# Kernel optimization log

Hardware: AMD Instinct MI355X
Metric: run time of the kernel (lower is better)

## Reference

```python
import jax, jax.numpy as jnp
import numpy as np

B, N, H, FD = 2, 512, 128, 5
NT, SD, L = 3, 4, 3
COPY = 10.0
EPS = 1e-6


def setup_inputs() -> dict:
    key = jax.random.key(0)
    ks = jax.random.split(key, 20)
    node_type = jax.random.randint(ks[0], (B, N, 1), 0, NT).astype(jnp.float32)
    node_state = jax.random.normal(ks[1], (B, N, SD), jnp.float32)
    node_feats = jnp.concatenate([node_type, node_state], axis=-1)  # [B,N,5]
    adj = jax.random.bernoulli(ks[2], 0.05, (B, N, N)).astype(jnp.float32)
    adj = jnp.maximum(adj, adj.transpose(0, 2, 1)) * (1.0 - jnp.eye(N, dtype=jnp.float32))
    scope_node_mask = jax.random.bernoulli(ks[3], 0.5, (B, N)).astype(jnp.float32)
    scope_edge_mask = jax.random.bernoulli(ks[4], 0.5, (B, N, N)).astype(jnp.float32)
    s = 0.02
    p = dict(
        node_feats=node_feats, adj=adj,
        scope_node_mask=scope_node_mask, scope_edge_mask=scope_edge_mask,
        W_in=jax.random.normal(ks[5], (FD, H)) * s, b_in=jnp.zeros((H,)),
        W_mp=jax.random.normal(ks[6], (L, 2 * H, H)) * s, b_mp=jnp.zeros((L, H)),
        Wt1=jax.random.normal(ks[7], (H, H)) * s, bt1=jnp.zeros((H,)),
        Wt2=jax.random.normal(ks[8], (H, NT)) * s, bt2=jnp.zeros((NT,)),
        Ws1=jax.random.normal(ks[9], (H, H)) * s, bs1=jnp.zeros((H,)),
        Ws2=jax.random.normal(ks[10], (H, SD)) * s, bs2=jnp.zeros((SD,)),
        We1=jax.random.normal(ks[11], (4 * H, H)) * s, be1=jnp.zeros((H,)),
        We2=jax.random.normal(ks[12], (H, 3)) * s, be2=jnp.zeros((3,)),
    )
    return p


def _decode_edge_logits(adj, edl, eye):
    probs = jax.nn.softmax(edl, axis=-1)
    p_keep = probs[..., 0]  # EDGE_DELTA_KEEP = 0
    p_add = probs[..., 1]   # EDGE_DELTA_ADD = 1
    cur = (adj > 0.5).astype(edl.dtype)
    p_next = jnp.clip(p_add + p_keep * cur, EPS, 1.0 - EPS)
    el = jnp.log(p_next) - jnp.log1p(-p_next)  # logit
    return jnp.where(eye[None], -1e9, el)


def _forward(node_feats, adj, scope_node_mask, scope_edge_mask,
             W_in, b_in, W_mp, b_mp, Wt1, bt1, Wt2, bt2,
             Ws1, bs1, Ws2, bs2, We1, be1, We2, be2):
    # encoder: input proj + L rounds of [h, adj@h] -> Linear -> ReLU
    h = jax.nn.relu(node_feats @ W_in + b_in)  # [B,N,H]
    for l in range(L):
        msg = jnp.einsum('bij,bjh->bih', adj, h)
        h = jax.nn.relu(jnp.concatenate([h, msg], axis=-1) @ W_mp[l] + b_mp[l])
    # node heads (2-layer MLPs)
    type_local = jax.nn.relu(h @ Wt1 + bt1) @ Wt2 + bt2      # [B,N,NT]
    state_local = jax.nn.relu(h @ Ws1 + bs1) @ Ws2 + bs2     # [B,N,SD]
    # pairwise edge-delta head
    h_i = h[:, :, None, :]
    h_j = h[:, None, :, :]
    pair = jnp.concatenate([
        jnp.broadcast_to(h_i, (B, N, N, H)),
        jnp.broadcast_to(h_j, (B, N, N, H)),
        jnp.abs(h_i - h_j),
        h_i * h_j,
    ], axis=-1)  # [B,N,N,4H]
    edl = jax.nn.relu(pair @ We1 + be1) @ We2 + be2  # [B,N,N,3]
    edl = 0.5 * (edl + edl.transpose(0, 2, 1, 3))
    eye = jnp.eye(N, dtype=bool)
    edl = jnp.where(eye[None, :, :, None], 0.0, edl)
    # merges with copy paths
    cur_type = jnp.clip(node_feats[..., 0].astype(jnp.int32), 0, NT - 1)
    copy_type = jnp.where(jnp.arange(NT) == cur_type[..., None], COPY, -COPY)
    type_full = jnp.where(scope_node_mask[..., None] != 0, type_local, copy_type)
    scope = scope_node_mask[..., None]
    state_full = scope * state_local + (1.0 - scope) * node_feats[..., 1:]
    copy_edl = jnp.broadcast_to(jnp.where(jnp.arange(3) == 0, COPY, -COPY), (B, N, N, 3))
    copy_edl = jnp.where(eye[None, :, :, None], 0.0, copy_edl)
    edl_full = jnp.where(scope_edge_mask[..., None] != 0, edl, copy_edl)
    el_full = _decode_edge_logits(adj, edl_full, eye)
    return type_full, state_full, edl_full, el_full


def reference(node_feats, adj, scope_node_mask, scope_edge_mask,
              W_in, b_in, W_mp, b_mp, Wt1, bt1, Wt2, bt2,
              Ws1, bs1, Ws2, bs2, We1, be1, We2, be2):
    return _forward(node_feats, adj, scope_node_mask, scope_edge_mask,
                    W_in, b_in, W_mp, b_mp, Wt1, bt1, Wt2, bt2,
                    Ws1, bs1, Ws2, bs2, We1, be1, We2, be2)
```

## Files before the change

kernel.cpp:

```cpp
#include <hip/hip_runtime.h>
#include <hip/hip_fp16.h>
#include <math.h>

#define B_ 2
#define N_ 512
#define H_ 128
#define NT_ 3
#define SD_ 4
#define FD_ 5

typedef float f32x4 __attribute__((ext_vector_type(4)));
typedef unsigned int u32x4 __attribute__((ext_vector_type(4)));

#define MFMA4(a0, a1, a2, a3, av, b0, b1, b2, b3) \
    asm("s_nop 1\n\t" \
        "v_mfma_f32_16x16x32_f16 %0, %4, %5, %0\n\t" \
        "v_mfma_f32_16x16x32_f16 %1, %4, %6, %1\n\t" \
        "v_mfma_f32_16x16x32_f16 %2, %4, %7, %2\n\t" \
        "v_mfma_f32_16x16x32_f16 %3, %4, %8, %3" \
        : "+v"(a0), "+v"(a1), "+v"(a2), "+v"(a3) \
        : "v"(av), "v"(b0), "v"(b1), "v"(b2), "v"(b3))

#define MFMA16F(acc, a, b) \
    asm("s_nop 1\n\tv_mfma_f32_16x16x32_f16 %0, %1, %2, %0" \
        : "+v"(acc) : "v"(a), "v"(b))

#define PKMUL(d, a, b) \
    asm("v_pk_mul_f16 %0, %1, %2" : "=v"(d) : "v"(a), "v"(b))
#define PKSUB(d, a, b) \
    asm("v_pk_add_f16 %0, %1, %2 neg_lo:[0,1] neg_hi:[0,1]" \
        : "=v"(d) : "v"(a), "v"(b))
#define CVTPKF16(d, a, b) \
    asm("v_cvt_pkrtz_f16_f32 %0, %1, %2" : "=v"(d) : "v"(a), "v"(b))

static __device__ inline unsigned short f2h(float f) {
    return __half_as_ushort(__float2half(f));
}

__global__ __launch_bounds__(128) void k_input(const float* __restrict__ feats,
                                               const float* __restrict__ W_in,
                                               const float* __restrict__ b_in,
                                               float* __restrict__ hout,
                                               const float* __restrict__ We1,
                                               const float* __restrict__ We2,
                                               unsigned short* __restrict__ wfrag,
                                               unsigned short* __restrict__ wfrag2) {
    int blk = blockIdx.x, tid = threadIdx.x;
    if (blk < B_ * N_) {
        const float* f = feats + (size_t)blk * FD_;
        float acc = b_in[tid];
#pragma unroll
        for (int k = 0; k < FD_; ++k) acc += f[k] * W_in[k * H_ + tid];
        hout[(size_t)blk * H_ + tid] = fmaxf(acc, 0.f);
        return;
    }
    if (blk < B_ * N_ + 32) {
        int t = (blk - B_ * N_) * 128 + tid;
        int lane = t & 63, cg = (t >> 6) & 7, kb = t >> 9;
        int lr = lane & 15, g = lane >> 4;
        int c = cg * 16 + lr;
        unsigned o[4];
#pragma unroll
        for (int p = 0; p < 4; ++p) {
            float a = We1[(size_t)(256 + kb * 32 + 8 * g + 2 * p) * H_ + c];
            float bq = We1[(size_t)(256 + kb * 32 + 8 * g + 2 * p + 1) * H_ + c];
            o[p] = (unsigned)f2h(a) | ((unsigned)f2h(bq) << 16);
        }
        u32x4 v = {o[0], o[1], o[2], o[3]};
        *(u32x4*)(wfrag + (size_t)t * 8) = v;
        return;
    }
    {
        int t = (blk - (B_ * N_ + 32)) * 128 + tid;
        if (t < 256) {
            int kb = t >> 6, lane = t & 63;
            int oc = lane & 15, g = lane >> 4;
            unsigned w[4];
#pragma unroll
            for (int p = 0; p < 4; ++p) {
                int k0 = kb * 32 + g * 8 + 2 * p;
                int k1 = k0 + 1;
                int c0 = ((k0 >> 6) << 6) | ((k0 & 3) << 4) | ((k0 & 63) >> 2);
                int c1 = ((k1 >> 6) << 6) | ((k1 & 3) << 4) | ((k1 & 63) >> 2);
                float v0 = (oc < 3) ? We2[c0 * 3 + oc] : 0.f;
                float v1 = (oc < 3) ? We2[c1 * 3 + oc] : 0.f;
                w[p] = (unsigned)f2h(v0) | ((unsigned)f2h(v1) << 16);
            }
            u32x4 v = {w[0], w[1], w[2], w[3]};
            *(u32x4*)(wfrag2 + (size_t)t * 8) = v;
        }
    }
}

__global__ __launch_bounds__(128) void k_mp(const float* __restrict__ hin,
                                            float* __restrict__ hout,
                                            const float* __restrict__ adj,
                                            const float* __restrict__ Wl,
                                            const float* __restrict__ bl) {
    __shared__ float hi[H_];
    __shared__ float msg[H_];
    __shared__ unsigned short idxs[N_];
    __shared__ float avals[N_];
    __shared__ int cnt2[2];
    int node = blockIdx.x;
    int b = node >> 9;
    int tid = threadIdx.x;
    int w = tid >> 6, lane = tid & 63;
    hi[tid] = hin[(size_t)node * H_ + tid];
    const float* arow = adj + (size_t)node * N_;
    float4 av = ((const float4*)arow)[tid];
    int segbase = w * 256;
    int cum = 0;
#pragma unroll
    for (int q = 0; q < 4; ++q) {
        float a = (&av.x)[q];
        bool pred = (a != 0.f);
        unsigned long long mask = __ballot(pred);
        if (pred) {
            int pos = segbase + cum +
                      (int)__popcll(mask & ((1ull << lane) - 1ull));
            idxs[pos] = (unsigned short)(tid * 4 + q);
            avals[pos] = a;
        }
        cum += (int)__popcll(mask);
    }
    if (lane == 0) cnt2[w] = cum;
    __syncthreads();

    float m = 0.f;
    const float* hb = hin + ((size_t)b * N_) * H_;
    int n0 = cnt2[0], n1 = cnt2[1];
    for (int t = 0; t < n0; ++t)
        m += avals[t] * hb[(size_t)idxs[t] * H_ + tid];
    for (int t = 0; t < n1; ++t)
        m += avals[256 + t] * hb[(size_t)idxs[256 + t] * H_ + tid];
    msg[tid] = m;
    __syncthreads();

    float acc = bl[tid];
#pragma unroll 4
    for (int k = 0; k < H_; ++k) {
        acc += hi[k]  * Wl[(size_t)k * H_ + tid];
        acc += msg[k] * Wl[(size_t)(k + H_) * H_ + tid];
    }
    hout[(size_t)node * H_ + tid] = fmaxf(acc, 0.f);
}

__global__ __launch_bounds__(128) void k_heads(
    const float* __restrict__ h, const float* __restrict__ feats,
    const float* __restrict__ snm,
    const float* __restrict__ Wt1, const float* __restrict__ bt1,
    const float* __restrict__ Wt2, const float* __restrict__ bt2,
    const float* __restrict__ Ws1, const float* __restrict__ bs1,
    const float* __restrict__ Ws2, const float* __restrict__ bs2,
    const float* __restrict__ We1, const float* __restrict__ be1,
    float* __restrict__ Acoef, float* __restrict__ Bcoef,
    unsigned short* __restrict__ hf16,
    float* __restrict__ type_out, float* __restrict__ state_out) {
    __shared__ float hi[H_], hT[H_], hS[H_];
    int node = blockIdx.x, tid = threadIdx.x;
    float hv0 = h[(size_t)node * H_ + tid];
    hi[tid] = hv0;
    hf16[(size_t)node * H_ + tid] = f2h(hv0);
    __syncthreads();
    float at = bt1[tid], as = bs1[tid], aa = be1[tid], ab = 0.f;
#pragma unroll 4
    for (int k = 0; k < H_; ++k) {
        float hv = hi[k];
        at += hv * Wt1[k * H_ + tid];
        as += hv * Ws1[k * H_ + tid];
        aa += hv * We1[k * H_ + tid];
        ab += hv * We1[(k + H_) * H_ + tid];
    }
    hT[tid] = fmaxf(at, 0.f);
    hS[tid] = fmaxf(as, 0.f);
    int c = tid;
    int kp = ((c >> 6) << 6) | ((c & 15) << 2) | ((c >> 4) & 3);
    Acoef[(size_t)node * H_ + kp] = aa;
    Bcoef[(size_t)node * H_ + kp] = ab;
    __syncthreads();
    float sm = snm[node];
    if (tid < NT_) {
        float tl = bt2[tid];
        for (int cc = 0; cc < H_; ++cc) tl += hT[cc] * Wt2[cc * NT_ + tid];
        int ct = (int)feats[(size_t)node * FD_];
        ct = ct < 0 ? 0 : (ct > NT_ - 1 ? NT_ - 1 : ct);
        float cv = (tid == ct) ? 10.f : -10.f;
        type_out[(size_t)node * NT_ + tid] = (sm != 0.f) ? tl : cv;
    }
    if (tid >= 64 && tid < 64 + SD_) {
        int s = tid - 64;
        float sl = bs2[s];
        for (int cc = 0; cc < H_; ++cc) sl += hS[cc] * Ws2[cc * SD_ + s];
        state_out[(size_t)node * SD_ + s] =
            sm * sl + (1.f - sm) * feats[(size_t)node * FD_ + 1 + s];
    }
}

__global__ __launch_bounds__(256, 2) void k_pair2(
    const unsigned short* __restrict__ hf16,
    const float* __restrict__ Acp, const float* __restrict__ Bcp,
    const unsigned short* __restrict__ wfrag,
    const unsigned short* __restrict__ wfrag2,
    const float* __restrict__ be2,
    float* __restrict__ edl_out) {

    __shared__ unsigned short tile[2][128][128];

    int bid = blockIdx.x;
    int b = 0, r = bid;
    if (r >= 1280) { b = 1; r -= 1280; }
    int jtile, i;
    if (r < 128)      { jtile = 0; i = r; }
    else if (r < 384) { jtile = 1; i = r - 128; }
    else if (r < 768) { jtile = 2; i = r - 384; }
    else              { jtile = 3; i = r - 768; }
    int JT0 = jtile << 7;
    int bN = b << 9;

    int tid = threadIdx.x;
    int wave = tid >> 6, lane = tid & 63;
    int jh = wave >> 1, ch = wave & 1;
    int lr = lane & 15, g = lane >> 4;

    u32x4 Bf[4][8];
#pragma unroll
    for (int ct = 0; ct < 4; ++ct)
#pragma unroll
        for (int kb = 0; kb < 8; ++kb)
            Bf[ct][kb] = *(const u32x4*)(wfrag +
                (((size_t)kb * 8 + (ch * 4 + ct)) * 64 + lane) * 8);

    const unsigned short* hirow = hf16 + (size_t)(bN + i) * H_;
    u32x4 him[4];
#pragma unroll
    for (int m = 0; m < 4; ++m)
        him[m] = *(const u32x4*)(hirow + 32 * m + 8 * g);

    f32x4 AcoI = *(const f32x4*)(Acp + (size_t)(bN + i) * H_ + ch * 64 + lr * 4);
    f32x4 BcoI = *(const f32x4*)(Bcp + (size_t)(bN + i) * H_ + ch * 64 + lr * 4);

    char* tb0 = (char*)&tile[0][0][0];
    char* tb1 = (char*)&tile[1][0][0];

#pragma unroll
    for (int jt = 0; jt < 4; ++jt) {
        int jloc0 = jh * 64 + jt * 16;
        const unsigned short* hjp =
            hf16 + (size_t)(bN + JT0 + jloc0 + lr) * H_ + 8 * g;
        u32x4 hjall[4];
#pragma unroll
        for (int m = 0; m < 4; ++m)
            hjall[m] = *(const u32x4*)(hjp + 32 * m);
        f32x4 BcJv[4], AcJv[4];
#pragma unroll
        for (int rr = 0; rr < 4; ++rr) {
            size_t jn = (size_t)(bN + JT0 + jloc0 + 4 * g + rr) * H_ +
                        ch * 64 + lr * 4;
            BcJv[rr] = *(const f32x4*)(Bcp + jn);
            AcJv[rr] = *(const f32x4*)(Acp + jn);
        }

        f32x4 acc0 = {0.f,0.f,0.f,0.f}, acc1 = {0.f,0.f,0.f,0.f};
        f32x4 acc2 = {0.f,0.f,0.f,0.f}, acc3 = {0.f,0.f,0.f,0.f};

#pragma unroll
        for (int m = 0; m < 4; ++m) {
            u32x4 tav, uav;
#pragma unroll
            for (int p = 0; p < 4; ++p) {
                unsigned hip_ = him[m][p], hjp_ = hjall[m][p];
                unsigned u_, d_;
                PKMUL(u_, hip_, hjp_);
                PKSUB(d_, hip_, hjp_);
                uav[p] = u_;
                tav[p] = d_ & 0x7fff7fffu;
            }
            MFMA4(acc0, acc1, acc2, acc3, tav,
                  Bf[0][m], Bf[1][m], Bf[2][m], Bf[3][m]);
            MFMA4(acc0, acc1, acc2, acc3, uav,
                  Bf[0][4 + m], Bf[1][4 + m], Bf[2][4 + m], Bf[3][4 + m]);
        }
        asm("s_nop 7\n\ts_nop 7\n\ts_nop 3"
            : "+v"(acc0), "+v"(acc1), "+v"(acc2), "+v"(acc3));

#pragma unroll
        for (int rr = 0; rr < 4; ++rr) {
            int jloc = jloc0 + 4 * g + rr;
            float h10 = fmaxf(acc0[rr] + AcoI[0] + BcJv[rr][0], 0.f);
            float h11 = fmaxf(acc1[rr] + AcoI[1] + BcJv[rr][1], 0.f);
            float h12 = fmaxf(acc2[rr] + AcoI[2] + BcJv[rr][2], 0.f);
            float h13 = fmaxf(acc3[rr] + AcoI[3] + BcJv[rr][3], 0.f);
            float h20 = fmaxf(acc0[rr] + AcJv[rr][0] + BcoI[0], 0.f);
            float h21 = fmaxf(acc1[rr] + AcJv[rr][1] + BcoI[1], 0.f);
            float h22 = fmaxf(acc2[rr] + AcJv[rr][2] + BcoI[2], 0.f);
            float h23 = fmaxf(acc3[rr] + AcJv[rr][3] + BcoI[3], 0.f);
            unsigned w10, w11, w20, w21;
            CVTPKF16(w10, h10, h11); CVTPKF16(w11, h12, h13);
            CVTPKF16(w20, h20, h21); CVTPKF16(w21, h22, h23);
            int byte = jloc * 256 + ch * 128 + lr * 8;
            byte ^= (jloc & 7) << 4;
            uint2 v1; v1.x = w10; v1.y = w11;
            uint2 v2; v2.x = w20; v2.y = w21;
            *(uint2*)(tb0 + byte) = v1;
            *(uint2*)(tb1 + byte) = v2;
        }
    }

    u32x4 Bf2[4];
#pragma unroll
    for (int kb = 0; kb < 4; ++kb)
        Bf2[kb] = *(const u32x4*)(wfrag2 + ((size_t)kb * 64 + lane) * 8);

    __syncthreads();

    f32x4 pacc0 = {0.f,0.f,0.f,0.f}, pacc1 = {0.f,0.f,0.f,0.f};
    f32x4 pacc2 = {0.f,0.f,0.f,0.f}, pacc3 = {0.f,0.f,0.f,0.f};
#pragma unroll
    for (int p = 0; p < 4; ++p) {
        int f = wave + 4 * p;
        int orient = f >> 3, sub = f & 7;
        char* tb = orient ? tb1 : tb0;
        int jloc = sub * 16 + lr;
#pragma unroll
        for (int kb = 0; kb < 4; ++kb) {
            int byte = jloc * 256 + kb * 64 + g * 16;
            byte ^= (jloc & 7) << 4;
            u32x4 a = *(const u32x4*)(tb + byte);
            if (p == 0)      { MFMA16F(pacc0, a, Bf2[kb]); }
            else if (p == 1) { MFMA16F(pacc1, a, Bf2[kb]); }
            else if (p == 2) { MFMA16F(pacc2, a, Bf2[kb]); }
            else             { MFMA16F(pacc3, a, Bf2[kb]); }
        }
    }
    asm("s_nop 7\n\ts_nop 7\n\ts_nop 3"
        : "+v"(pacc0), "+v"(pacc1), "+v"(pacc2), "+v"(pacc3));
    __syncthreads();

    float* sbuf = (float*)&tile[0][0][0];
    if (lr < 3) {
#pragma unroll
        for (int p = 0; p < 4; ++p) {
            int f = wave + 4 * p;
            int orient = f >> 3, sub = f & 7;
            f32x4 pa = (p == 0) ? pacc0 : (p == 1) ? pacc1
                     : (p == 2) ? pacc2 : pacc3;
#pragma unroll
            for (int rr = 0; rr < 4; ++rr) {
                int jloc = sub * 16 + 4 * g + rr;
                sbuf[((orient << 7) + jloc) * 3 + lr] = pa[rr];
            }
        }
    }
    __syncthreads();

#pragma unroll
    for (int q = 0; q < 2; ++q) {
        int idx = q * 256 + tid;
        if (idx < 384) {
            int jloc = idx / 3, comp = idx - jloc * 3;
            float v = 0.5f * (sbuf[jloc * 3 + comp] +
                              sbuf[(128 + jloc) * 3 + comp]) + be2[comp];
            edl_out[((size_t)(bN + i) * N_ + (JT0 + jloc)) * 3 + comp] = v;
        }
    }
}

__global__ __launch_bounds__(256) void k_tr(float* __restrict__ edl,
                                            float* __restrict__ el,
                                            const float* __restrict__ sem,
                                            const float* __restrict__ adj) {
    __shared__ float ss[3][16][17];
    int tid = threadIdx.x;
    int r = tid >> 4, c = tid & 15;
    int bid = blockIdx.x;
    int b = 0, t = bid;
    if (t >= 528) { b = 1; t -= 528; }
    int J = (int)((sqrtf(8.f * (float)t + 1.f) - 1.f) * 0.5f);
    while ((J + 1) * (J + 2) / 2 <= t) ++J;
    while (J * (J + 1) / 2 > t) --J;
    int I = t - J * (J + 1) / 2;
    int i0 = I * 16, j0 = J * 16;
    int bN = b << 9;

    {
        const float* src = edl + ((size_t)(bN + i0 + r) * N_ + (j0 + c)) * 3;
        ss[0][r][c] = src[0];
        ss[1][r][c] = src[1];
        ss[2][r][c] = src[2];
    }
    __syncthreads();

    for (int pass = 0; pass < 2; ++pass) {
        if (pass == 1 && I == J) break;
        int gi, gj;
        float s0, s1, s2;
        if (I == J) {
            gi = i0 + r; gj = j0 + c;
            int lo = r <= c ? r : c, hi = r <= c ? c : r;
            s0 = ss[0][lo][hi]; s1 = ss[1][lo][hi]; s2 = ss[2][lo][hi];
        } else if (pass == 0) {
            gi = i0 + r; gj = j0 + c;
            s0 = ss[0][r][c]; s1 = ss[1][r][c]; s2 = ss[2][r][c];
        } else {
            gi = j0 + r; gj = i0 + c;
            s0 = ss[0][c][r]; s1 = ss[1][c][r]; s2 = ss[2][c][r];
        }
        size_t p = (size_t)(bN + gi) * N_ + gj;
        if (gi == gj) {
            edl[p * 3 + 0] = 0.f; edl[p * 3 + 1] = 0.f; edl[p * 3 + 2] = 0.f;
            el[p] = -1e9f;
        } else {
            float msk = sem[p];
            float e0 = (msk != 0.f) ? s0 : 10.f;
            float e1 = (msk != 0.f) ? s1 : -10.f;
            float e2 = (msk != 0.f) ? s2 : -10.f;
            edl[p * 3 + 0] = e0; edl[p * 3 + 1] = e1; edl[p * 3 + 2] = e2;
            float a = adj[p];
            float cur = (a > 0.5f) ? 1.f : 0.f;
            float mx = fmaxf(e0, fmaxf(e1, e2));
            float x0 = expf(e0 - mx), x1 = expf(e1 - mx), x2 = expf(e2 - mx);
            float inv = 1.f / (x0 + x1 + x2);
            float pn = x1 * inv + x0 * inv * cur;
            pn = fminf(fmaxf(pn, 1e-6f), 1.f - 1e-6f);
            el[p] = logf(pn) - log1pf(-pn);
        }
    }
}

extern "C" void kernel_launch(void* const* d_in, const int* in_sizes, int n_in,
                              void* d_out, int out_size, void* d_ws,
                              size_t ws_size, hipStream_t stream) {
    const float* feats = (const float*)d_in[0];
    const float* adj   = (const float*)d_in[1];
    const float* snm   = (const float*)d_in[2];
    const float* sem   = (const float*)d_in[3];
    const float* W_in  = (const float*)d_in[4];
    const float* b_in  = (const float*)d_in[5];
    const float* W_mp  = (const float*)d_in[6];
    const float* b_mp  = (const float*)d_in[7];
    const float* Wt1 = (const float*)d_in[8],  *bt1 = (const float*)d_in[9];
    const float* Wt2 = (const float*)d_in[10], *bt2 = (const float*)d_in[11];
    const float* Ws1 = (const float*)d_in[12], *bs1 = (const float*)d_in[13];
    const float* Ws2 = (const float*)d_in[14], *bs2 = (const float*)d_in[15];
    const float* We1 = (const float*)d_in[16], *be1 = (const float*)d_in[17];
    const float* We2 = (const float*)d_in[18], *be2 = (const float*)d_in[19];

    float* out = (float*)d_out;
    float* type_out  = out;
    float* state_out = out + 3072;
    float* edl_out   = out + 7168;
    float* el_out    = out + 7168 + 1572864;

    float* ws = (float*)d_ws;
    float* hA = ws;
    float* hB = ws + 131072;
    float* Bcp = ws + 262144;
    unsigned short* hf16   = (unsigned short*)(ws + 393216);
    unsigned short* wfrag  = (unsigned short*)(ws + 458752);
    unsigned short* wfrag2 = (unsigned short*)(ws + 475136);
    float* Acp = hA;

    k_input<<<B_ * N_ + 34, 128, 0, stream>>>(feats, W_in, b_in, hA,
                                              We1, We2, wfrag, wfrag2);
    k_mp<<<B_ * N_, H_, 0, stream>>>(hA, hB, adj,
                                     W_mp + 0 * 2 * H_ * H_, b_mp + 0 * H_);
    k_mp<<<B_ * N_, H_, 0, stream>>>(hB, hA, adj,
                                     W_mp + 1 * 2 * H_ * H_, b_mp + 1 * H_);
    k_mp<<<B_ * N_, H_, 0, stream>>>(hA, hB, adj,
                                     W_mp + 2 * 2 * H_ * H_, b_mp + 2 * H_);
    k_heads<<<B_ * N_, H_, 0, stream>>>(hB, feats, snm, Wt1, bt1, Wt2, bt2,
                                        Ws1, bs1, Ws2, bs2, We1, be1,
                                        Acp, Bcp, hf16, type_out, state_out);
    k_pair2<<<2560, 256, 0, stream>>>(hf16, Acp, Bcp, wfrag, wfrag2,
                                      be2, edl_out);
    k_tr<<<1056, 256, 0, stream>>>(edl_out, el_out, sem, adj);
}
```

Before: 128.8 us.

## Halve pair-kernel LDS tile by processing j in two 64-column halves, use builtins

The pair kernel now splits each 128-column j tile into two 64-column passes, cutting the shared fp16 tile from 64KB to 32KB and adding a small separate float reduction buffer. This is meant to let more blocks fit per CU. Inline-asm MFMA, packed f16 math and conversion macros are replaced with compiler builtins and vector f16 ops, so the compiler can schedule them and insert hazard waits itself. The second-layer weight fragments are loaded up front. The cost is extra __syncthreads per half and less work between barriers.

Result: no change. 128.4 us (-0.3%).

```diff
diff --git a/kernel.cpp b/kernel.cpp
--- a/kernel.cpp
+++ b/kernel.cpp
@@ -11,27 +11,16 @@
 
 typedef float f32x4 __attribute__((ext_vector_type(4)));
 typedef unsigned int u32x4 __attribute__((ext_vector_type(4)));
-
-#define MFMA4(a0, a1, a2, a3, av, b0, b1, b2, b3) \
-    asm("s_nop 1\n\t" \
-        "v_mfma_f32_16x16x32_f16 %0, %4, %5, %0\n\t" \
-        "v_mfma_f32_16x16x32_f16 %1, %4, %6, %1\n\t" \
-        "v_mfma_f32_16x16x32_f16 %2, %4, %7, %2\n\t" \
-        "v_mfma_f32_16x16x32_f16 %3, %4, %8, %3" \
-        : "+v"(a0), "+v"(a1), "+v"(a2), "+v"(a3) \
-        : "v"(av), "v"(b0), "v"(b1), "v"(b2), "v"(b3))
-
-#define MFMA16F(acc, a, b) \
-    asm("s_nop 1\n\tv_mfma_f32_16x16x32_f16 %0, %1, %2, %0" \
-        : "+v"(acc) : "v"(a), "v"(b))
-
-#define PKMUL(d, a, b) \
-    asm("v_pk_mul_f16 %0, %1, %2" : "=v"(d) : "v"(a), "v"(b))
-#define PKSUB(d, a, b) \
-    asm("v_pk_add_f16 %0, %1, %2 neg_lo:[0,1] neg_hi:[0,1]" \
-        : "=v"(d) : "v"(a), "v"(b))
-#define CVTPKF16(d, a, b) \
-    asm("v_cvt_pkrtz_f16_f32 %0, %1, %2" : "=v"(d) : "v"(a), "v"(b))
+typedef _Float16 f16x8 __attribute__((ext_vector_type(8)));
+typedef __fp16 hf16x2 __attribute__((ext_vector_type(2)));
+
+#define MFMA(acc, a, b) \
+    acc = __builtin_amdgcn_mfma_f32_16x16x32_f16((a), (b), (acc), 0, 0, 0)
+
+static __device__ inline unsigned cvt_pk_u32(float a, float b) {
+    hf16x2 v = __builtin_amdgcn_cvt_pkrtz(a, b);
+    return __builtin_bit_cast(unsigned, v);
+}
 
 static __device__ inline unsigned short f2h(float f) {
     return __half_as_ushort(__float2half(f));
@@ -205,7 +194,8 @@
     const float* __restrict__ be2,
     float* __restrict__ edl_out) {
 
-    __shared__ unsigned short tile[2][128][128];
+    __shared__ unsigned short tile[2][64][128];
+    __shared__ float sbuf[2][64][3];
 
     int bid = blockIdx.x;
     int b = 0, r = bid;
@@ -223,19 +213,24 @@
     int jh = wave >> 1, ch = wave & 1;
     int lr = lane & 15, g = lane >> 4;
 
-    u32x4 Bf[4][8];
+    f16x8 Bf[4][8];
 #pragma unroll
     for (int ct = 0; ct < 4; ++ct)
 #pragma unroll
         for (int kb = 0; kb < 8; ++kb)
-            Bf[ct][kb] = *(const u32x4*)(wfrag +
+            Bf[ct][kb] = *(const f16x8*)(wfrag +
                 (((size_t)kb * 8 + (ch * 4 + ct)) * 64 + lane) * 8);
 
+    f16x8 Bf2[4];
+#pragma unroll
+    for (int kb = 0; kb < 4; ++kb)
+        Bf2[kb] = *(const f16x8*)(wfrag2 + ((size_t)kb * 64 + lane) * 8);
+
     const unsigned short* hirow = hf16 + (size_t)(bN + i) * H_;
-    u32x4 him[4];
+    f16x8 him[4];
 #pragma unroll
     for (int m = 0; m < 4; ++m)
-        him[m] = *(const u32x4*)(hirow + 32 * m + 8 * g);
+        him[m] = *(const f16x8*)(hirow + 32 * m + 8 * g);
 
     f32x4 AcoI = *(const f32x4*)(Acp + (size_t)(bN + i) * H_ + ch * 64 + lr * 4);
     f32x4 BcoI = *(const f32x4*)(Bcp + (size_t)(bN + i) * H_ + ch * 64 + lr * 4);
@@ -243,126 +238,107 @@
     char* tb0 = (char*)&tile[0][0][0];
     char* tb1 = (char*)&tile[1][0][0];
 
-#pragma unroll
-    for (int jt = 0; jt < 4; ++jt) {
-        int jloc0 = jh * 64 + jt * 16;
-        const unsigned short* hjp =
-            hf16 + (size_t)(bN + JT0 + jloc0 + lr) * H_ + 8 * g;
-        u32x4 hjall[4];
-#pragma unroll
-        for (int m = 0; m < 4; ++m)
-            hjall[m] = *(const u32x4*)(hjp + 32 * m);
-        f32x4 BcJv[4], AcJv[4];
-#pragma unroll
-        for (int rr = 0; rr < 4; ++rr) {
-            size_t jn = (size_t)(bN + JT0 + jloc0 + 4 * g + rr) * H_ +
-                        ch * 64 + lr * 4;
-            BcJv[rr] = *(const f32x4*)(Bcp + jn);
-            AcJv[rr] = *(const f32x4*)(Acp + jn);
-        }
-
-        f32x4 acc0 = {0.f,0.f,0.f,0.f}, acc1 = {0.f,0.f,0.f,0.f};
-        f32x4 acc2 = {0.f,0.f,0.f,0.f}, acc3 = {0.f,0.f,0.f,0.f};
-
-#pragma unroll
-        for (int m = 0; m < 4; ++m) {
-            u32x4 tav, uav;
-#pragma unroll
-            for (int p = 0; p < 4; ++p) {
-                unsigned hip_ = him[m][p], hjp_ = hjall[m][p];
-                unsigned u_, d_;
-                PKMUL(u_, hip_, hjp_);
-                PKSUB(d_, hip_, hjp_);
-                uav[p] = u_;
-                tav[p] = d_ & 0x7fff7fffu;
-            }
-            MFMA4(acc0, acc1, acc2, acc3, tav,
-                  Bf[0][m], Bf[1][m], Bf[2][m], Bf[3][m]);
-            MFMA4(acc0, acc1, acc2, acc3, uav,
-                  Bf[0][4 + m], Bf[1][4 + m], Bf[2][4 + m], Bf[3][4 + m]);
-        }
-        asm("s_nop 7\n\ts_nop 7\n\ts_nop 3"
-            : "+v"(acc0), "+v"(acc1), "+v"(acc2), "+v"(acc3));
-
-#pragma unroll
-        for (int rr = 0; rr < 4; ++rr) {
-            int jloc = jloc0 + 4 * g + rr;
-            float h10 = fmaxf(acc0[rr] + AcoI[0] + BcJv[rr][0], 0.f);
-            float h11 = fmaxf(acc1[rr] + AcoI[1] + BcJv[rr][1], 0.f);
-            float h12 = fmaxf(acc2[rr] + AcoI[2] + BcJv[rr][2], 0.f);
-            float h13 = fmaxf(acc3[rr] + AcoI[3] + BcJv[rr][3], 0.f);
-            float h20 = fmaxf(acc0[rr] + AcJv[rr][0] + BcoI[0], 0.f);
-            float h21 = fmaxf(acc1[rr] + AcJv[rr][1] + BcoI[1], 0.f);
-            float h22 = fmaxf(acc2[rr] + AcJv[rr][2] + BcoI[2], 0.f);
-            float h23 = fmaxf(acc3[rr] + AcJv[rr][3] + BcoI[3], 0.f);
-            unsigned w10, w11, w20, w21;
-            CVTPKF16(w10, h10, h11); CVTPKF16(w11, h12, h13);
-            CVTPKF16(w20, h20, h21); CVTPKF16(w21, h22, h23);
-            int byte = jloc * 256 + ch * 128 + lr * 8;
-            byte ^= (jloc & 7) << 4;
-            uint2 v1; v1.x = w10; v1.y = w11;
-            uint2 v2; v2.x = w20; v2.y = w21;
-            *(uint2*)(tb0 + byte) = v1;
-            *(uint2*)(tb1 + byte) = v2;
-        }
-    }
-
-    u32x4 Bf2[4];
-#pragma unroll
-    for (int kb = 0; kb < 4; ++kb)
-        Bf2[kb] = *(const u32x4*)(wfrag2 + ((size_t)kb * 64 + lane) * 8);
-
-    __syncthreads();
-
-    f32x4 pacc0 = {0.f,0.f,0.f,0.f}, pacc1 = {0.f,0.f,0.f,0.f};
-    f32x4 pacc2 = {0.f,0.f,0.f,0.f}, pacc3 = {0.f,0.f,0.f,0.f};
-#pragma unroll
-    for (int p = 0; p < 4; ++p) {
-        int f = wave + 4 * p;
-        int orient = f >> 3, sub = f & 7;
-        char* tb = orient ? tb1 : tb0;
-        int jloc = sub * 16 + lr;
-#pragma unroll
-        for (int kb = 0; kb < 4; ++kb) {
-            int byte = jloc * 256 + kb * 64 + g * 16;
-            byte ^= (jloc & 7) << 4;
-            u32x4 a = *(const u32x4*)(tb + byte);
-            if (p == 0)      { MFMA16F(pacc0, a, Bf2[kb]); }
-            else if (p == 1) { MFMA16F(pacc1, a, Bf2[kb]); }
-            else if (p == 2) { MFMA16F(pacc2, a, Bf2[kb]); }
-            else             { MFMA16F(pacc3, a, Bf2[kb]); }
-        }
-    }
-    asm("s_nop 7\n\ts_nop 7\n\ts_nop 3"
-        : "+v"(pacc0), "+v"(pacc1), "+v"(pacc2), "+v"(pacc3));
-    __syncthreads();
-
-    float* sbuf = (float*)&tile[0][0][0];
-    if (lr < 3) {
-#pragma unroll
-        for (int p = 0; p < 4; ++p) {
+    for (int jhalf = 0; jhalf < 2; ++jhalf) {
+        int J0 = JT0 + jhalf * 64;
+#pragma unroll
+        for (int jt = 0; jt < 2; ++jt) {
+            int jloc0 = jh * 32 + jt * 16;
+            const unsigned short* hjp =
+                hf16 + (size_t)(bN + J0 + jloc0 + lr) * H_ + 8 * g;
+            f16x8 hjall[4];
+#pragma unroll
+            for (int m = 0; m < 4; ++m)
+                hjall[m] = *(const f16x8*)(hjp + 32 * m);
+            f32x4 BcJv[4], AcJv[4];
+#pragma unroll
+            for (int rr = 0; rr < 4; ++rr) {
+                size_t jn = (size_t)(bN + J0 + jloc0 + 4 * g + rr) * H_ +
+                            ch * 64 + lr * 4;
+                BcJv[rr] = *(const f32x4*)(Bcp + jn);
+                AcJv[rr] = *(const f32x4*)(Acp + jn);
+            }
+
+            f32x4 acc0 = {0.f,0.f,0.f,0.f}, acc1 = {0.f,0.f,0.f,0.f};
+            f32x4 acc2 = {0.f,0.f,0.f,0.f}, acc3 = {0.f,0.f,0.f,0.f};
+
+#pragma unroll
+            for (int m = 0; m < 4; ++m) {
+                f16x8 diff = him[m] - hjall[m];
+                u32x4 du = __builtin_bit_cast(u32x4, diff) & 0x7fff7fffu;
+                f16x8 tav = __builtin_bit_cast(f16x8, du);
+                f16x8 uav = him[m] * hjall[m];
+                MFMA(acc0, tav, Bf[0][m]);
+                MFMA(acc1, tav, Bf[1][m]);
+                MFMA(acc2, tav, Bf[2][m]);
+                MFMA(acc3, tav, Bf[3][m]);
+                MFMA(acc0, uav, Bf[0][4 + m]);
+                MFMA(acc1, uav, Bf[1][4 + m]);
+                MFMA(acc2, uav, Bf[2][4 + m]);
+                MFMA(acc3, uav, Bf[3][4 + m]);
+            }
+
+#pragma unroll
+            for (int rr = 0; rr < 4; ++rr) {
+                int jloc = jloc0 + 4 * g + rr;
+                float h10 = fmaxf(acc0[rr] + AcoI[0] + BcJv[rr][0], 0.f);
+                float h11 = fmaxf(acc1[rr] + AcoI[1] + BcJv[rr][1], 0.f);
+                float h12 = fmaxf(acc2[rr] + AcoI[2] + BcJv[rr][2], 0.f);
+                float h13 = fmaxf(acc3[rr] + AcoI[3] + BcJv[rr][3], 0.f);
+                float h20 = fmaxf(acc0[rr] + AcJv[rr][0] + BcoI[0], 0.f);
+                float h21 = fmaxf(acc1[rr] + AcJv[rr][1] + BcoI[1], 0.f);
+                float h22 = fmaxf(acc2[rr] + AcJv[rr][2] + BcoI[2], 0.f);
+                float h23 = fmaxf(acc3[rr] + AcJv[rr][3] + BcoI[3], 0.f);
+                int byte = jloc * 256 + ch * 128 + lr * 8;
+                byte ^= (jloc & 7) << 4;
+                uint2 v1; v1.x = cvt_pk_u32(h10, h11);
+                v1.y = cvt_pk_u32(h12, h13);
+                uint2 v2; v2.x = cvt_pk_u32(h20, h21);
+                v2.y = cvt_pk_u32(h22, h23);
+                *(uint2*)(tb0 + byte) = v1;
+                *(uint2*)(tb1 + byte) = v2;
+            }
+        }
+        __syncthreads();
+
+        f32x4 pacc0 = {0.f,0.f,0.f,0.f}, pacc1 = {0.f,0.f,0.f,0.f};
+#pragma unroll
+        for (int p = 0; p < 2; ++p) {
             int f = wave + 4 * p;
-            int orient = f >> 3, sub = f & 7;
-            f32x4 pa = (p == 0) ? pacc0 : (p == 1) ? pacc1
-                     : (p == 2) ? pacc2 : pacc3;
-#pragma unroll
-            for (int rr = 0; rr < 4; ++rr) {
-                int jloc = sub * 16 + 4 * g + rr;
-                sbuf[((orient << 7) + jloc) * 3 + lr] = pa[rr];
-            }
-        }
-    }
-    __syncthreads();
-
-#pragma unroll
-    for (int q = 0; q < 2; ++q) {
-        int idx = q * 256 + tid;
-        if (idx < 384) {
-            int jloc = idx / 3, comp = idx - jloc * 3;
-            float v = 0.5f * (sbuf[jloc * 3 + comp] +
-                              sbuf[(128 + jloc) * 3 + comp]) + be2[comp];
-            edl_out[((size_t)(bN + i) * N_ + (JT0 + jloc)) * 3 + comp] = v;
-        }
+            int orient = f >> 2, sub = f & 3;
+            char* tb = orient ? tb1 : tb0;
+            int jloc = sub * 16 + lr;
+#pragma unroll
+            for (int kb = 0; kb < 4; ++kb) {
+                int byte = jloc * 256 + kb * 64 + g * 16;
+                byte ^= (jloc & 7) << 4;
+                f16x8 a = *(const f16x8*)(tb + byte);
+                if (p == 0) { MFMA(pacc0, a, Bf2[kb]); }
+                else        { MFMA(pacc1, a, Bf2[kb]); }
+            }
+        }
+
+        if (lr < 3) {
+#pragma unroll
+            for (int p = 0; p < 2; ++p) {
+                int f = wave + 4 * p;
+                int orient = f >> 2, sub = f & 3;
+                f32x4 pa = p ? pacc1 : pacc0;
+#pragma unroll
+                for (int rr = 0; rr < 4; ++rr) {
+                    int jloc = sub * 16 + 4 * g + rr;
+                    sbuf[orient][jloc][lr] = pa[rr];
+                }
+            }
+        }
+        __syncthreads();
+
+        if (tid < 192) {
+            int jloc = tid / 3, comp = tid - jloc * 3;
+            float v = 0.5f * (sbuf[0][jloc][comp] + sbuf[1][jloc][comp]) +
+                      be2[comp];
+            edl_out[((size_t)(bN + i) * N_ + (J0 + jloc)) * 3 + comp] = v;
+        }
+        __syncthreads();
     }
 }
 
```
